# Optimization experiments

Hardware: AMD Instinct MI355X
Metric: run time of the kernel (lower is better)

Reference implementation:

```python
import jax, jax.numpy as jnp
import numpy as np

B, NQ, S, D = 8, 1024, 2048, 512

def setup_inputs() -> dict:
    key = jax.random.key(0)
    k1, k2, k3, k4 = jax.random.split(key, 4)
    queries = jax.random.normal(k1, (B, NQ, D), dtype=jnp.float32)
    keys = jax.random.normal(k2, (B, S, D), dtype=jnp.float32)
    values = jax.random.normal(k3, (B, S, D), dtype=jnp.float32)
    mask = jax.random.randint(k4, (B, NQ, S), 0, 2, dtype=jnp.int32)
    return {"queries": queries, "keys": keys, "values": values, "mask": mask}

def reference(queries, keys, values, mask):
    # scores: dot-product attention scores (b, nq, s)
    scores = jnp.einsum('bqd,bsd->bqs', queries, keys)
    attention_dist = jax.nn.softmax(scores, axis=2)
    # mask then renormalize over seq axis
    attention_dist = attention_dist * mask.astype(attention_dist.dtype)
    attention_dist = attention_dist / attention_dist.sum(axis=2, keepdims=True)
    # weighted sum of values: equivalent to (dist.unsqueeze(3) * values.unsqueeze(1)).sum(2)
    final_vector = jnp.einsum('bqs,bsd->bqd', attention_dist, values)
    return final_vector
```

## Files before the change

### kernel.cpp

```cpp
#include <hip/hip_runtime.h>


#define Bz 8
#define NQz 1024
#define Sz 2048
#define Dz 512
#define QT 32
#define TS 32
#define NT ((Sz / 2) / TS)
#define KP 520
#define PP 40

typedef _Float16 f16x8 __attribute__((ext_vector_type(8)));
typedef float f32x4 __attribute__((ext_vector_type(4)));
typedef unsigned short ushort_t;

#define AS1(p) ((const __attribute__((address_space(1))) unsigned int*)(p))
#define AS3(p) ((__attribute__((address_space(3))) unsigned int*)(p))
#define DRAIN_ALL() __builtin_amdgcn_s_waitcnt(0)

__device__ __forceinline__ ushort_t f2h(float x) {
  _Float16 h = (_Float16)x;
  return __builtin_bit_cast(ushort_t, h);
}
__device__ __forceinline__ float h2f(ushort_t u) {
  return (float)__builtin_bit_cast(_Float16, u);
}

__global__ __launch_bounds__(256)
void prep(const float* __restrict__ K, const float* __restrict__ V,
          ushort_t* __restrict__ Kf, ushort_t* __restrict__ Vt) {
  __shared__ ushort_t sT[32][72];
  const int t = threadIdx.x;
  int bx = blockIdx.x;
  if (bx < 8192) {
    size_t e = ((size_t)bx * 256 + t) * 4;
    float4 v = *(const float4*)(K + e);
    uint2 w;
    w.x = (unsigned)f2h(v.x) | ((unsigned)f2h(v.y) << 16);
    w.y = (unsigned)f2h(v.z) | ((unsigned)f2h(v.w) << 16);
    *(uint2*)(Kf + e) = w;
    return;
  }
  bx -= 8192;
  const int b = bx >> 9;
  const int rest = bx & 511;
  const int st = rest >> 3;
  const int dt = rest & 7;
  const int s0 = st * 32, d0 = dt * 64;
  const float* Vb = V + ((size_t)b * Sz + s0) * Dz + d0;
#pragma unroll
  for (int i = 0; i < 2; ++i) {
    int idx = t + 256 * i;
    int s = idx >> 4;
    int dc = (idx & 15) * 4;
    float4 v = *(const float4*)(Vb + (size_t)s * Dz + dc);
    uint2 w;
    w.x = (unsigned)f2h(v.x) | ((unsigned)f2h(v.y) << 16);
    w.y = (unsigned)f2h(v.z) | ((unsigned)f2h(v.w) << 16);
    *(uint2*)(&sT[s][dc]) = w;
  }
  __syncthreads();
  ushort_t* VtB = Vt + ((size_t)b * Dz + d0) * Sz + s0;
  {
    int d = t >> 2, c = t & 3;
    uint4 u;
    ushort_t* tp = (ushort_t*)&u;
#pragma unroll
    for (int j = 0; j < 8; ++j) tp[j] = sT[c * 8 + j][d];
    *(uint4*)(VtB + (size_t)d * Sz + c * 8) = u;
  }
}

__global__ __launch_bounds__(256, 2)
void attn_flash(const float* __restrict__ Q, const int* __restrict__ Msk,
                const ushort_t* __restrict__ Kf, const ushort_t* __restrict__ Vt,
                float* __restrict__ Opart, float* __restrict__ Mpart,
                float* __restrict__ Lpart) {
  __shared__ ushort_t sK[TS][KP];
  __shared__ ushort_t sV[Dz][TS];
  __shared__ ushort_t sP[QT][PP];
  __shared__ float sTMax[2][QT];
  __shared__ float sTSum[2][QT];
  __shared__ float sM[2][QT];
  __shared__ float sL[2][QT];

  const int tid  = threadIdx.x;
  const int wave = tid >> 6;
  const int lane = tid & 63;
  const int l16  = lane & 15;
  const int quad = lane >> 4;
  const int rw   = wave & 1;
  const int cw   = wave >> 1;

  const int bx = blockIdx.x;
  const int b  = bx >> 6;
  const int r6 = bx & 63;
  const int qt = r6 >> 1;
  const int sh = r6 & 1;
  const int q0 = qt * QT;
  const int sbeg = sh * (Sz / 2);

  const float*    Qb  = Q  + ((size_t)b * NQz + q0) * Dz;
  const ushort_t* KfB = Kf + (size_t)b * Sz * Dz;
  const ushort_t* VtB = Vt + (size_t)b * Dz * Sz;
  const int*      Mb  = Msk + ((size_t)b * NQz + q0) * (size_t)Sz;

  int msk_r[4];

  auto issue_k = [&](int s0n) {
#pragma unroll
    for (int j = 0; j < 8; ++j) {
      int row = wave * 8 + j;
      const ushort_t* gp = KfB + (size_t)(s0n + row) * Dz + lane * 8;
      __builtin_amdgcn_global_load_lds(AS1(gp), AS3(&sK[row][0]), 16, 0, 0);
    }
  };
  auto issue_v = [&](int s0n) {
#pragma unroll
    for (int j = 0; j < 8; ++j) {
      int dbase = wave * 128 + j * 16;
      const ushort_t* gp =
          VtB + (size_t)(dbase + (lane >> 2)) * Sz + s0n + (lane & 3) * 8;
      __builtin_amdgcn_global_load_lds(AS1(gp), AS3(&sV[dbase][0]), 16, 0, 0);
    }
  };
  auto load_mask = [&](int s0n) {
#pragma unroll
    for (int r = 0; r < 4; ++r) {
      int qrow = rw * 16 + quad * 4 + r;
      msk_r[r] = Mb[(size_t)qrow * Sz + s0n + cw * 16 + l16];
    }
  };

  issue_k(sbeg);
  load_mask(sbeg);

  f16x8 qa[16];
  {
    const float* qrow = Qb + (size_t)(rw * 16 + l16) * Dz;
#pragma unroll
    for (int kk = 0; kk < 16; ++kk) {
      const float4 a = *(const float4*)(qrow + kk * 32 + quad * 8);
      const float4 c = *(const float4*)(qrow + kk * 32 + quad * 8 + 4);
      f16x8 h;
      h[0] = (_Float16)a.x; h[1] = (_Float16)a.y;
      h[2] = (_Float16)a.z; h[3] = (_Float16)a.w;
      h[4] = (_Float16)c.x; h[5] = (_Float16)c.y;
      h[6] = (_Float16)c.z; h[7] = (_Float16)c.w;
      qa[kk] = h;
    }
  }

  if (tid < QT) { sM[0][tid] = -1e30f; sL[0][tid] = 0.0f; }

  f32x4 oacc[16];
#pragma unroll
  for (int t = 0; t < 16; ++t) oacc[t] = (f32x4){0.f, 0.f, 0.f, 0.f};

  int p = 0;
  for (int i = 0; i < NT; ++i) {
    const int s0 = sbeg + i * TS;
    const int sNext = (i + 1 < NT) ? s0 + TS : sbeg;

    DRAIN_ALL();
    __syncthreads();

    issue_v(s0);

    f32x4 sc = (f32x4){0.f, 0.f, 0.f, 0.f};
    {
      const ushort_t* kh = &sK[cw * 16 + l16][quad * 8];
#pragma unroll
      for (int kk = 0; kk < 16; ++kk) {
        f16x8 bh = *(const f16x8*)(kh + kk * 32);
        sc = __builtin_amdgcn_mfma_f32_16x16x32_f16(qa[kk], bh, sc, 0, 0, 0);
      }
    }

    float se[4];
#pragma unroll
    for (int r = 0; r < 4; ++r) se[r] = msk_r[r] ? sc[r] : -1e30f;
    float rmax[4] = {se[0], se[1], se[2], se[3]};
#pragma unroll
    for (int d = 1; d < 16; d <<= 1) {
#pragma unroll
      for (int r = 0; r < 4; ++r) rmax[r] = fmaxf(rmax[r], __shfl_xor(rmax[r], d));
    }
    float rsum[4];
#pragma unroll
    for (int r = 0; r < 4; ++r) {
      int row = rw * 16 + quad * 4 + r;
      float pv = msk_r[r] ? __expf(sc[r] - rmax[r]) : 0.0f;
      ushort_t pb = f2h(pv);
      sP[row][cw * 16 + l16] = pb;
      rsum[r] = h2f(pb);
    }
#pragma unroll
    for (int d = 1; d < 16; d <<= 1) {
#pragma unroll
      for (int r = 0; r < 4; ++r) rsum[r] += __shfl_xor(rsum[r], d);
    }
    if (l16 == 0) {
#pragma unroll
      for (int r = 0; r < 4; ++r) {
        int row = rw * 16 + quad * 4 + r;
        sTMax[cw][row] = rmax[r];
        sTSum[cw][row] = rsum[r];
      }
    }

    DRAIN_ALL();
    __syncthreads();

    issue_k(sNext);
    load_mask(sNext);

    const int pr = p;
    {
      const int row16 = rw * 16 + l16;
      float t0v = sTMax[0][row16], t1v = sTMax[1][row16];
      float mo16 = sM[pr][row16];
      float mn16 = fmaxf(mo16, fmaxf(t0v, t1v));
      float scl = __expf(((quad >> 1) ? t1v : t0v) - mn16);
      f16x8 praw = *(const f16x8*)(&sP[row16][quad * 8]);
      f16x8 pa;
#pragma unroll
      for (int j = 0; j < 8; ++j) pa[j] = (_Float16)((float)praw[j] * scl);

      float alpha[4];
#pragma unroll
      for (int r = 0; r < 4; ++r) {
        int rc = rw * 16 + quad * 4 + r;
        float a0 = sTMax[0][rc], a1 = sTMax[1][rc];
        float mo = sM[pr][rc];
        float mn = fmaxf(mo, fmaxf(a0, a1));
        float al = __expf(mo - mn);
        alpha[r] = al;
        if (cw == 0 && l16 == 0) {
          sM[pr ^ 1][rc] = mn;
          sL[pr ^ 1][rc] = al * sL[pr][rc] + __expf(a0 - mn) * sTSum[0][rc]
                                           + __expf(a1 - mn) * sTSum[1][rc];
        }
      }
#pragma unroll
      for (int t = 0; t < 16; ++t) {
#pragma unroll
        for (int r = 0; r < 4; ++r) oacc[t][r] *= alpha[r];
      }
#pragma unroll
      for (int t = 0; t < 16; ++t) {
        f16x8 vb = *(const f16x8*)(&sV[cw * 256 + t * 16 + l16][quad * 8]);
        oacc[t] = __builtin_amdgcn_mfma_f32_16x16x32_f16(pa, vb, oacc[t], 0, 0, 0);
      }
    }
    p ^= 1;
  }

  DRAIN_ALL();
  __syncthreads();
  const size_t rbase = (size_t)(b * 2 + sh) * NQz + q0;
#pragma unroll
  for (int t = 0; t < 16; ++t) {
#pragma unroll
    for (int r = 0; r < 4; ++r) {
      int rowq = rw * 16 + quad * 4 + r;
      Opart[(rbase + rowq) * Dz + cw * 256 + t * 16 + l16] = oacc[t][r];
    }
  }
  if (tid < QT) {
    Mpart[rbase + tid] = sM[p][tid];
    Lpart[rbase + tid] = sL[p][tid];
  }
}

__global__ __launch_bounds__(256)
void combine(const float* __restrict__ Opart, const float* __restrict__ Mpart,
             const float* __restrict__ Lpart, float* __restrict__ Out) {
  int gid = blockIdx.x * 256 + threadIdx.x;
  int row = gid >> 7;
  int b   = row >> 10;
  int q   = row & 1023;
  int c   = (gid & 127) * 4;
  size_t i0 = (size_t)(b * 2 + 0) * NQz + q;
  size_t i1 = (size_t)(b * 2 + 1) * NQz + q;
  float m0 = Mpart[i0], m1 = Mpart[i1];
  float l0 = Lpart[i0], l1 = Lpart[i1];
  float m  = fmaxf(m0, m1);
  float w0 = __expf(m0 - m), w1 = __expf(m1 - m);
  float inv = 1.0f / (w0 * l0 + w1 * l1);
  float4 a = *(const float4*)(Opart + i0 * Dz + c);
  float4 bv = *(const float4*)(Opart + i1 * Dz + c);
  float4 o;
  o.x = (w0 * a.x + w1 * bv.x) * inv;
  o.y = (w0 * a.y + w1 * bv.y) * inv;
  o.z = (w0 * a.z + w1 * bv.z) * inv;
  o.w = (w0 * a.w + w1 * bv.w) * inv;
  *(float4*)(Out + ((size_t)b * NQz + q) * Dz + c) = o;
}

extern "C" void kernel_launch(void* const* d_in, const int* in_sizes, int n_in,
                              void* d_out, int out_size, void* d_ws, size_t ws_size,
                              hipStream_t stream) {
  const float* Q = (const float*)d_in[0];
  const float* K = (const float*)d_in[1];
  const float* V = (const float*)d_in[2];
  const int*   M = (const int*)d_in[3];
  float* O = (float*)d_out;

  const size_t NKV = (size_t)Bz * Sz * Dz;
  ushort_t* Kf = (ushort_t*)d_ws;
  ushort_t* Vt = Kf + NKV;
  float* Opart = (float*)(Vt + NKV);
  float* Mpart = Opart + (size_t)Bz * 2 * NQz * Dz;
  float* Lpart = Mpart + (size_t)Bz * 2 * NQz;

  prep<<<dim3(12288), dim3(256), 0, stream>>>(K, V, Kf, Vt);
  attn_flash<<<dim3(512), dim3(256), 0, stream>>>(Q, M, Kf, Vt, Opart, Mpart, Lpart);
  combine<<<dim3(4096), dim3(256), 0, stream>>>(Opart, Mpart, Lpart, O);
}
```

Baseline: 270.7 us.

## Transpose QK^T MFMA so score rows lie along lanes and vectorize mask loads

Swaps the MFMA operands so each lane holds four consecutive key columns of a single query row. The row max and row sum then need only two cross-lane shuffles instead of four rounds over four registers. The mask is read as one int4 per lane, and the P tile is written to shared memory as one packed 8-byte store. The dot-product chain is also split into two independent accumulators to cut MFMA dependency stalls, at the cost of an extra add and a few more registers.

```diff
diff --git a/kernel.cpp b/kernel.cpp
--- a/kernel.cpp
+++ b/kernel.cpp
@@ -126,11 +126,9 @@
     }
   };
   auto load_mask = [&](int s0n) {
-#pragma unroll
-    for (int r = 0; r < 4; ++r) {
-      int qrow = rw * 16 + quad * 4 + r;
-      msk_r[r] = Mb[(size_t)qrow * Sz + s0n + cw * 16 + l16];
-    }
+    const int4 mv = *(const int4*)(Mb + (size_t)(rw * 16 + l16) * Sz + s0n +
+                                   cw * 16 + quad * 4);
+    msk_r[0] = mv.x; msk_r[1] = mv.y; msk_r[2] = mv.z; msk_r[3] = mv.w;
   };
 
   issue_k(sbeg);
@@ -168,46 +166,47 @@
 
     issue_v(s0);
 
-    f32x4 sc = (f32x4){0.f, 0.f, 0.f, 0.f};
+    f32x4 sc0 = (f32x4){0.f, 0.f, 0.f, 0.f};
+    f32x4 sc1 = (f32x4){0.f, 0.f, 0.f, 0.f};
     {
       const ushort_t* kh = &sK[cw * 16 + l16][quad * 8];
 #pragma unroll
-      for (int kk = 0; kk < 16; ++kk) {
-        f16x8 bh = *(const f16x8*)(kh + kk * 32);
-        sc = __builtin_amdgcn_mfma_f32_16x16x32_f16(qa[kk], bh, sc, 0, 0, 0);
+      for (int kk = 0; kk < 16; kk += 2) {
+        f16x8 b0 = *(const f16x8*)(kh + kk * 32);
+        f16x8 b1 = *(const f16x8*)(kh + kk * 32 + 32);
+        sc0 = __builtin_amdgcn_mfma_f32_16x16x32_f16(b0, qa[kk], sc0, 0, 0, 0);
+        sc1 = __builtin_amdgcn_mfma_f32_16x16x32_f16(b1, qa[kk + 1], sc1, 0, 0, 0);
       }
     }
+    f32x4 sc;
+#pragma unroll
+    for (int r = 0; r < 4; ++r) sc[r] = sc0[r] + sc1[r];
 
     float se[4];
 #pragma unroll
     for (int r = 0; r < 4; ++r) se[r] = msk_r[r] ? sc[r] : -1e30f;
-    float rmax[4] = {se[0], se[1], se[2], se[3]};
-#pragma unroll
-    for (int d = 1; d < 16; d <<= 1) {
-#pragma unroll
-      for (int r = 0; r < 4; ++r) rmax[r] = fmaxf(rmax[r], __shfl_xor(rmax[r], d));
-    }
-    float rsum[4];
+    float rmax = fmaxf(fmaxf(se[0], se[1]), fmaxf(se[2], se[3]));
+    rmax = fmaxf(rmax, __shfl_xor(rmax, 16));
+    rmax = fmaxf(rmax, __shfl_xor(rmax, 32));
+    ushort_t pb[4];
+    float rsum = 0.f;
 #pragma unroll
     for (int r = 0; r < 4; ++r) {
-      int row = rw * 16 + quad * 4 + r;
-      float pv = msk_r[r] ? __expf(sc[r] - rmax[r]) : 0.0f;
-      ushort_t pb = f2h(pv);
-      sP[row][cw * 16 + l16] = pb;
-      rsum[r] = h2f(pb);
-    }
-#pragma unroll
-    for (int d = 1; d < 16; d <<= 1) {
-#pragma unroll
-      for (int r = 0; r < 4; ++r) rsum[r] += __shfl_xor(rsum[r], d);
-    }
-    if (l16 == 0) {
-#pragma unroll
-      for (int r = 0; r < 4; ++r) {
-        int row = rw * 16 + quad * 4 + r;
-        sTMax[cw][row] = rmax[r];
-        sTSum[cw][row] = rsum[r];
-      }
+      float pv = msk_r[r] ? __expf(se[r] - rmax) : 0.0f;
+      pb[r] = f2h(pv);
+      rsum += h2f(pb[r]);
+    }
+    {
+      uint2 w;
+      w.x = (unsigned)pb[0] | ((unsigned)pb[1] << 16);
+      w.y = (unsigned)pb[2] | ((unsigned)pb[3] << 16);
+      *(uint2*)(&sP[rw * 16 + l16][cw * 16 + quad * 4]) = w;
+    }
+    rsum += __shfl_xor(rsum, 16);
+    rsum += __shfl_xor(rsum, 32);
+    if (quad == 0) {
+      sTMax[cw][rw * 16 + l16] = rmax;
+      sTSum[cw][rw * 16 + l16] = rsum;
     }
 
     DRAIN_ALL();
```

Result: faster. 257.2 us (-5.0%).
